# Kernel tuning notes

Measured on AMD Instinct MI355X. Metric: run time of the kernel, lower is better.

The kernel has to match this reference:

```python
import jax, jax.numpy as jnp
import numpy as np
import math

DIM = 384
NUM_HEADS = 12
WS = 8  # window_size


def setup_inputs() -> dict:
    key = jax.random.key(0)
    k1, k2, k3 = jax.random.split(key, 3)
    B, N, C = 16, 4096, DIM
    x = jax.random.normal(k1, (B, N, C), dtype=jnp.float32)
    W_qkv = jax.random.normal(k2, (C, 3 * C), dtype=jnp.float32) * 0.02
    b_qkv = jnp.zeros((3 * C,), dtype=jnp.float32)
    W_proj = jax.random.normal(k3, (C, C), dtype=jnp.float32) * 0.02
    return {"x": x, "W_qkv": W_qkv, "b_qkv": b_qkv, "W_proj": W_proj}


def window_attention(x, W_qkv, b_qkv, W_proj):
    B, N, C = x.shape
    H = W = int(math.isqrt(N))
    nh = NUM_HEADS
    hd = C // nh
    scale = hd ** (-0.5)
    ws = WS
    pad_h = (ws - H % ws) % ws
    pad_w = (ws - W % ws) % ws
    xg = x.reshape(B, H, W, C)
    if pad_h or pad_w:
        xg = jnp.pad(xg, ((0, 0), (0, pad_h), (0, pad_w), (0, 0)))
    Hp, Wp = H + pad_h, W + pad_w
    nH, nW = Hp // ws, Wp // ws
    # partition into windows: [B, nWin, ws*ws, C]
    xw = xg.reshape(B, nH, ws, nW, ws, C).transpose(0, 1, 3, 2, 4, 5)
    xw = xw.reshape(B, nH * nW, ws * ws, C)
    # qkv projection
    qkv = xw @ W_qkv + b_qkv  # [B, nWin, ws2, 3C]
    qkv = qkv.reshape(B, nH * nW, ws * ws, 3, nh, hd)
    q = qkv[..., 0, :, :].transpose(0, 1, 3, 2, 4)  # [B, nWin, nh, ws2, hd]
    k = qkv[..., 1, :, :].transpose(0, 1, 3, 2, 4)
    v = qkv[..., 2, :, :].transpose(0, 1, 3, 2, 4)
    attn = jnp.einsum('bwhqd,bwhkd->bwhqk', q, k) * scale
    attn = jax.nn.softmax(attn, axis=-1)
    out = jnp.einsum('bwhqk,bwhkd->bwhqd', attn, v)
    out = out.transpose(0, 1, 3, 2, 4).reshape(B, nH * nW, ws * ws, C)
    out = out @ W_proj
    # un-partition windows
    out = out.reshape(B, nH, nW, ws, ws, C).transpose(0, 1, 3, 2, 4, 5)
    out = out.reshape(B, Hp, Wp, C)
    if pad_h or pad_w:
        out = out[:, :H, :W, :]
    return out.reshape(B, H * W, C)


def reference(x, W_qkv, b_qkv, W_proj):
    return window_attention(x, W_qkv, b_qkv, W_proj)
```

## Files before the change

### kernel.cpp

```cpp
#include <hip/hip_runtime.h>
#include <hip/hip_bf16.h>


typedef _Float16 f16;
typedef f16 f16x8 __attribute__((ext_vector_type(8)));
typedef f16 f16x4 __attribute__((ext_vector_type(4)));
typedef float f32x4 __attribute__((ext_vector_type(4)));

#define MFMA_F16(a, b, c) __builtin_amdgcn_mfma_f32_16x16x32_f16((a), (b), (c), 0, 0, 0)

#define AS_G __attribute__((address_space(1)))
#define AS_L __attribute__((address_space(3)))
#define GLOAD_LDS16(gp, lp) \
  __builtin_amdgcn_global_load_lds((const AS_G void*)(gp), (AS_L void*)(lp), 16, 0, 0)
#define WAITVM_(N) asm volatile("s_waitcnt vmcnt(" #N ")" ::: "memory")
#define WAITVM(N) WAITVM_(N)

namespace {
constexpr int kC = 384;
constexpr int kNTok = 4096;
constexpr float kScale = 0.17677669529663687f;
constexpr int kWqPackChunks = 72 * 12 * 64;
constexpr int kWpPackChunks = 24 * 12 * 64;
constexpr size_t kWqPackBytes = (size_t)kWqPackChunks * 16;
constexpr size_t kWpPackBytes = (size_t)kWpPackChunks * 16;
constexpr size_t kQkvWsBytes = (size_t)65536 * 1152 * 2;
constexpr size_t kWsNeed = kWqPackBytes + kWpPackBytes + kQkvWsBytes;
constexpr int kQkvPackChunksFb = 6 * 12 * 12 * 64;
}


__global__ void prep_weights_split(const float* __restrict__ Wqkv,
                                   const float* __restrict__ Wproj,
                                   f16* __restrict__ wq_pack,
                                   f16* __restrict__ wp_pack) {
  int i = blockIdx.x * 256 + threadIdx.x;
  if (i < kWqPackChunks) {
    int lane = i & 63;
    int chunk = i >> 6;
    int ks = chunk % 12;
    int t = chunk / 12;
    int l15 = lane & 15, g = lane >> 4;
    int n3 = t * 16 + l15;
    int k0 = ks * 32 + g * 8;
    f16x8 v;
    #pragma unroll
    for (int j = 0; j < 8; ++j)
      v[j] = (f16)Wqkv[(size_t)(k0 + j) * (3 * kC) + n3];
    *reinterpret_cast<f16x8*>(wq_pack + (size_t)i * 8) = v;
  } else if (i < kWqPackChunks + kWpPackChunks) {
    int p = i - kWqPackChunks;
    int lane = p & 63;
    int chunk = p >> 6;
    int ks = chunk % 12;
    int t = chunk / 12;
    int l15 = lane & 15, g = lane >> 4;
    int n = t * 16 + l15;
    int k0 = ks * 32 + g * 8;
    f16x8 v;
    #pragma unroll
    for (int j = 0; j < 8; ++j)
      v[j] = (f16)Wproj[(size_t)(k0 + j) * kC + n];
    *reinterpret_cast<f16x8*>(wp_pack + (size_t)p * 8) = v;
  }
}

__global__ void prep_x(const float* __restrict__ x, f16* __restrict__ xw) {
  int c = blockIdx.x * 256 + threadIdx.x;
  int lane = c & 63;
  int t = c >> 6;
  int ks = t % 12;
  int mb = t / 12;
  int l15 = lane & 15, g = lane >> 4;
  int m = mb * 16 + l15;
  int b = m >> 12;
  int win = (m >> 6) & 63;
  int tok = m & 63;
  int n = ((win >> 3) * 8 + (tok >> 3)) * 64 + (win & 7) * 8 + (tok & 7);
  const float* src = x + ((size_t)(b << 12) + n) * kC + ks * 32 + g * 8;
  float4 v0 = *reinterpret_cast<const float4*>(src);
  float4 v1 = *reinterpret_cast<const float4*>(src + 4);
  f16x8 h = {(f16)v0.x, (f16)v0.y, (f16)v0.z, (f16)v0.w,
             (f16)v1.x, (f16)v1.y, (f16)v1.z, (f16)v1.w};
  *reinterpret_cast<f16x8*>(xw + (size_t)c * 8) = h;
}

__global__ __launch_bounds__(256, 3) void qkv_gemm2(
    const f16* __restrict__ xw, const float* __restrict__ b_qkv,
    const f16* __restrict__ wq_pack, f16* __restrict__ qkv_ws) {
  __shared__ alignas(1024) char smem[49152];

  const int tid = threadIdx.x;
  const int wid = tid >> 6;
  const int lane = tid & 63;
  const int g = lane >> 4;
  const int l15 = lane & 15;
  const int wm = wid >> 1;
  const int wn = wid & 1;

  int bid = blockIdx.x;
  int wg = (bid & 7) * 576 + (bid >> 3);
  int m_grp = wg / 9;
  int n_grp = wg - m_grp * 9;
  const int mb0 = m_grp * 8;
  const int nb0 = n_grp * 8;

  #define STAGE(KS, BUF)                                                     \
    do {                                                                     \
      const f16* ga0 = xw + (((size_t)(mb0 + wid) * 12 + (KS)) * 64 + lane) * 8;     \
      const f16* ga1 = xw + (((size_t)(mb0 + 4 + wid) * 12 + (KS)) * 64 + lane) * 8; \
      const f16* gb0 =                                                       \
          wq_pack + (((size_t)(nb0 + wid) * 12 + (KS)) * 64 + lane) * 8;     \
      const f16* gb1 =                                                       \
          wq_pack + (((size_t)(nb0 + 4 + wid) * 12 + (KS)) * 64 + lane) * 8; \
      char* la = smem + (BUF) * 16384 + wid * 1024;                          \
      char* lb = smem + (BUF) * 16384 + 8192 + wid * 1024;                   \
      GLOAD_LDS16(ga0, la);                                                  \
      GLOAD_LDS16(ga1, la + 4096);                                           \
      GLOAD_LDS16(gb0, lb);                                                  \
      GLOAD_LDS16(gb1, lb + 4096);                                           \
    } while (0)

  f32x4 acc[4][4];
  #pragma unroll
  for (int mt = 0; mt < 4; ++mt)
    #pragma unroll
    for (int nt = 0; nt < 4; ++nt) acc[mt][nt] = {0.f, 0.f, 0.f, 0.f};

  STAGE(0, 0);
  STAGE(1, 1);
  STAGE(2, 2);
  WAITVM(8);
  __builtin_amdgcn_sched_barrier(0);
  __builtin_amdgcn_s_barrier();

  #define KITER(T, ENDVM)                                                    \
    do {                                                                     \
      constexpr int buf = (T) % 3;                                           \
      f16x8 af[4], bf[4];                                                    \
      _Pragma("unroll") for (int mt = 0; mt < 4; ++mt) af[mt] =              \
          *reinterpret_cast<const f16x8*>(smem + buf * 16384 +               \
                                          (wm * 4 + mt) * 1024 + lane * 16); \
      _Pragma("unroll") for (int nt = 0; nt < 4; ++nt) bf[nt] =              \
          *reinterpret_cast<const f16x8*>(smem + buf * 16384 + 8192 +        \
                                          (wn * 4 + nt) * 1024 + lane * 16); \
      asm volatile("s_waitcnt lgkmcnt(0)" ::: "memory");                     \
      __builtin_amdgcn_sched_barrier(0);                                     \
      __builtin_amdgcn_s_barrier();                                          \
      if ((T) < 9) {                                                         \
        STAGE((T) + 3, buf);                                                 \
      }                                                                      \
      __builtin_amdgcn_s_setprio(1);                                         \
      _Pragma("unroll") for (int mt = 0; mt < 4; ++mt)                       \
          _Pragma("unroll") for (int nt = 0; nt < 4; ++nt) acc[mt][nt] =     \
          MFMA_F16(af[mt], bf[nt], acc[mt][nt]);                             \
      __builtin_amdgcn_s_setprio(0);                                         \
      WAITVM(ENDVM);                                                         \
      __builtin_amdgcn_sched_barrier(0);                                     \
      __builtin_amdgcn_s_barrier();                                          \
    } while (0)

  KITER(0, 8);
  KITER(1, 8);
  KITER(2, 8);
  KITER(3, 8);
  KITER(4, 8);
  KITER(5, 8);
  KITER(6, 8);
  KITER(7, 8);
  KITER(8, 8);
  KITER(9, 4);
  KITER(10, 0);
  KITER(11, 0);
  #undef KITER
  #undef STAGE

  f16* eo = (f16*)smem;
  #pragma unroll
  for (int nt = 0; nt < 4; ++nt) {
    int col128 = wn * 64 + nt * 16 + l15;
    float bias = b_qkv[n_grp * 128 + col128];
    int hsec_loc = col128 >> 5;
    int d = col128 & 31;
    #pragma unroll
    for (int mt = 0; mt < 4; ++mt) {
      #pragma unroll
      for (int j = 0; j < 4; ++j) {
        int tok = mt * 16 + g * 4 + j;
        eo[(((wm * 4 + hsec_loc) * 64) + tok) * 32 + d] =
            (f16)(acc[mt][nt][j] + bias);
      }
    }
  }
  __syncthreads();
  #pragma unroll
  for (int i = 0; i < 8; ++i) {
    int u = tid + i * 256;
    int win_loc = u >> 10;
    int cbl = (u >> 8) & 3;
    int inner = u & 255;
    int cb = n_grp * 4 + cbl;
    int h = cb % 12;
    int sec = cb / 12;
    size_t dst = ((size_t)(m_grp * 2 + win_loc) * 36 + h * 3 + sec) * 2048 +
                 (size_t)inner * 8;
    *reinterpret_cast<f16x8*>(qkv_ws + dst) =
        *reinterpret_cast<const f16x8*>(eo + (size_t)u * 8);
  }
}

__global__ __launch_bounds__(512, 4) void attn_proj(
    const f16* __restrict__ qkv_ws, const f16* __restrict__ wp_pack,
    float* __restrict__ out) {
  __shared__ alignas(16) f16 ao[64][392];
  __shared__ alignas(16) f16 vT[2][32][72];
  __shared__ alignas(16) f16 p_s[8][16][72];

  const int tid = threadIdx.x;
  const int wid = tid >> 6;
  const int lane = tid & 63;
  const int g = lane >> 4;
  const int l15 = lane & 15;
  const int wm = wid >> 2;
  const int wn = wid & 3;

  const int blk = blockIdx.x;
  const int b = blk >> 6;
  const int win = blk & 63;
  const int wh = win >> 3;
  const int ww = win & 7;

  const f32x4 zero4 = {0.f, 0.f, 0.f, 0.f};
  const f16* qkvb = qkv_ws + (size_t)(b * 64 + win) * 36 * 2048;

  const int v_hh = tid >> 8;
  const int v_tok = (tid >> 2) & 63;
  const int v_d0 = (tid & 3) * 8;

  for (int hp = 0; hp < 6; ++hp) {
    {
      int h2 = 2 * hp + v_hh;
      f16x8 v = *reinterpret_cast<const f16x8*>(
          qkvb + ((size_t)(h2 * 3 + 2) * 64 + v_tok) * 32 + v_d0);
      #pragma unroll
      for (int j = 0; j < 8; ++j) vT[v_hh][v_d0 + j][v_tok] = v[j];
    }
    __syncthreads();

    const int h = 2 * hp + wm;
    const f16* hb = qkvb + (size_t)h * 3 * 2048;
    f16x8 qa =
        *reinterpret_cast<const f16x8*>(hb + (wn * 16 + l15) * 32 + g * 8);
    f32x4 sacc[4];
    #pragma unroll
    for (int nt = 0; nt < 4; ++nt) sacc[nt] = zero4;
    #pragma unroll
    for (int nt = 0; nt < 4; ++nt) {
      f16x8 kb = *reinterpret_cast<const f16x8*>(
          hb + 2048 + (nt * 16 + l15) * 32 + g * 8);
      sacc[nt] = MFMA_F16(qa, kb, sacc[nt]);
    }

    float pv[4][4];
    #pragma unroll
    for (int j = 0; j < 4; ++j) {
      float m = -1e30f;
      #pragma unroll
      for (int nt = 0; nt < 4; ++nt) {
        pv[nt][j] = sacc[nt][j] * kScale;
        m = fmaxf(m, pv[nt][j]);
      }
      m = fmaxf(m, __shfl_xor(m, 1));
      m = fmaxf(m, __shfl_xor(m, 2));
      m = fmaxf(m, __shfl_xor(m, 4));
      m = fmaxf(m, __shfl_xor(m, 8));
      float s = 0.f;
      #pragma unroll
      for (int nt = 0; nt < 4; ++nt) {
        pv[nt][j] = __expf(pv[nt][j] - m);
        s += pv[nt][j];
      }
      s += __shfl_xor(s, 1);
      s += __shfl_xor(s, 2);
      s += __shfl_xor(s, 4);
      s += __shfl_xor(s, 8);
      float inv = 1.0f / s;
      #pragma unroll
      for (int nt = 0; nt < 4; ++nt)
        p_s[wid][g * 4 + j][nt * 16 + l15] = (f16)(pv[nt][j] * inv);
    }

    f32x4 oacc[2];
    oacc[0] = zero4;
    oacc[1] = zero4;
    #pragma unroll
    for (int ks = 0; ks < 2; ++ks) {
      f16x8 pa =
          *reinterpret_cast<const f16x8*>(&p_s[wid][l15][ks * 32 + g * 8]);
      #pragma unroll
      for (int nt = 0; nt < 2; ++nt) {
        f16x8 vb = *reinterpret_cast<const f16x8*>(
            &vT[wm][nt * 16 + l15][ks * 32 + g * 8]);
        oacc[nt] = MFMA_F16(pa, vb, oacc[nt]);
      }
    }
    #pragma unroll
    for (int nt = 0; nt < 2; ++nt)
      #pragma unroll
      for (int j = 0; j < 4; ++j)
        ao[wn * 16 + g * 4 + j][h * 32 + nt * 16 + l15] = (f16)oacc[nt][j];
    __syncthreads();
  }

  f32x4 pacc[2][6];
  #pragma unroll
  for (int mt = 0; mt < 2; ++mt)
    #pragma unroll
    for (int nt = 0; nt < 6; ++nt) pacc[mt][nt] = zero4;

  const f16* pptr[6];
  #pragma unroll
  for (int nt = 0; nt < 6; ++nt) {
    int t = wn * 6 + nt;
    pptr[nt] = wp_pack + ((size_t)(t * 12) * 64 + lane) * 8;
  }
  f16x8 pbf[2][6];
  #pragma unroll
  for (int nt = 0; nt < 6; ++nt)
    pbf[0][nt] = *reinterpret_cast<const f16x8*>(pptr[nt]);

  #pragma unroll
  for (int ks = 0; ks < 12; ++ks) {
    const int cur = ks & 1;
    if (ks < 11) {
      #pragma unroll
      for (int nt = 0; nt < 6; ++nt)
        pbf[cur ^ 1][nt] =
            *reinterpret_cast<const f16x8*>(pptr[nt] + (ks + 1) * 512);
    }
    f16x8 paf[2];
    #pragma unroll
    for (int mt = 0; mt < 2; ++mt)
      paf[mt] = *reinterpret_cast<const f16x8*>(
          &ao[wm * 32 + mt * 16 + l15][ks * 32 + g * 8]);
    #pragma unroll
    for (int mt = 0; mt < 2; ++mt)
      #pragma unroll
      for (int nt = 0; nt < 6; ++nt)
        pacc[mt][nt] = MFMA_F16(paf[mt], pbf[cur][nt], pacc[mt][nt]);
  }

  const size_t outbase = (size_t)b * kNTok * kC;
  #pragma unroll
  for (int mt = 0; mt < 2; ++mt) {
    #pragma unroll
    for (int j = 0; j < 4; ++j) {
      int r = wm * 32 + mt * 16 + g * 4 + j;
      int n = (wh * 8 + (r >> 3)) * 64 + ww * 8 + (r & 7);
      float* orow = out + outbase + (size_t)n * kC + wn * 96;
      #pragma unroll
      for (int nt = 0; nt < 6; ++nt) orow[nt * 16 + l15] = pacc[mt][nt][j];
    }
  }
}


__global__ void prep_weights_fb(const float* __restrict__ Wqkv,
                                const float* __restrict__ Wproj,
                                f16* __restrict__ wq_pack,
                                f16* __restrict__ wp_pack) {
  int i = blockIdx.x * 256 + threadIdx.x;
  if (i < kQkvPackChunksFb) {
    int lane = i & 63;
    int chunk = i >> 6;
    int ks = chunk % 12;
    int t = (chunk / 12) % 12;
    int hp = chunk / 144;
    int l15 = lane & 15, g = lane >> 4;
    int base = t * 16;
    int hh = base / 96;
    int cc = base - hh * 96;
    int sec = cc >> 5;
    int dbhi = cc & 31;
    int n3 = sec * kC + (2 * hp + hh) * 32 + dbhi + l15;
    int k0 = ks * 32 + g * 8;
    f16x8 v;
    #pragma unroll
    for (int j = 0; j < 8; ++j)
      v[j] = (f16)Wqkv[(size_t)(k0 + j) * (3 * kC) + n3];
    *reinterpret_cast<f16x8*>(wq_pack + (size_t)i * 8) = v;
  } else if (i < kQkvPackChunksFb + kWpPackChunks) {
    int p = i - kQkvPackChunksFb;
    int lane = p & 63;
    int chunk = p >> 6;
    int ks = chunk % 12;
    int t = chunk / 12;
    int l15 = lane & 15, g = lane >> 4;
    int n = t * 16 + l15;
    int k0 = ks * 32 + g * 8;
    f16x8 v;
    #pragma unroll
    for (int j = 0; j < 8; ++j)
      v[j] = (f16)Wproj[(size_t)(k0 + j) * kC + n];
    *reinterpret_cast<f16x8*>(wp_pack + (size_t)p * 8) = v;
  }
}

__global__ __launch_bounds__(512, 2) void win_attn_fused_fb(
    const float* __restrict__ x, const float* __restrict__ b_qkv,
    const f16* __restrict__ wq_pack, const f16* __restrict__ wp_pack,
    float* __restrict__ out) {
  __shared__ alignas(16) f16 xs[64][392];
  __shared__ alignas(16) f16 ao[64][392];
  __shared__ alignas(16) f16 q_s[2][64][40];
  __shared__ alignas(16) f16 k_s[2][64][40];
  __shared__ alignas(16) f16 vT[2][32][72];
  __shared__ alignas(16) f16 p_s[8][16][72];

  const int tid = threadIdx.x;
  const int wid = tid >> 6;
  const int lane = tid & 63;
  const int g = lane >> 4;
  const int l15 = lane & 15;
  const int wm = wid >> 2;
  const int wn = wid & 3;

  const int blk = blockIdx.x;
  const int b = blk >> 6;
  const int win = blk & 63;
  const int wh = win >> 3;
  const int ww = win & 7;

  const f32x4 zero4 = {0.f, 0.f, 0.f, 0.f};

  {
    const float* xb = x + (size_t)b * kNTok * kC;
    #pragma unroll
    for (int it = 0; it < 12; ++it) {
      int idx = tid + it * 512;
      int r = idx / 96;
      int c4 = idx - r * 96;
      int n = (wh * 8 + (r >> 3)) * 64 + ww * 8 + (r & 7);
      float4 v = *reinterpret_cast<const float4*>(xb + (size_t)n * kC + c4 * 4);
      f16x4 hv = {(f16)v.x, (f16)v.y, (f16)v.z, (f16)v.w};
      *reinterpret_cast<f16x4*>(&xs[r][c4 * 4]) = hv;
    }
  }
  __syncthreads();

  for (int hp = 0; hp < 6; ++hp) {
    f32x4 acc[2][3];
    #pragma unroll
    for (int mt = 0; mt < 2; ++mt)
      #pragma unroll
      for (int nt = 0; nt < 3; ++nt) acc[mt][nt] = zero4;

    const f16* bptr[3];
    int secv[3], dbv[3], hhv[3];
    #pragma unroll
    for (int nt = 0; nt < 3; ++nt) {
      int t = wn * 3 + nt;
      int base = t * 16;
      int hh = base / 96;
      int cc = base - hh * 96;
      hhv[nt] = hh;
      secv[nt] = cc >> 5;
      dbv[nt] = cc & 31;
      bptr[nt] = wq_pack + ((size_t)((hp * 12 + t) * 12) * 64 + lane) * 8;
    }

    f16x8 bf[4][3];
    f16x8 af[2][2];
    #pragma unroll
    for (int p = 0; p < 3; ++p)
      #pragma unroll
      for (int nt = 0; nt < 3; ++nt)
        bf[p][nt] = *reinterpret_cast<const f16x8*>(bptr[nt] + p * 512);
    #pragma unroll
    for (int mt = 0; mt < 2; ++mt)
      af[0][mt] = *reinterpret_cast<const f16x8*>(
          &xs[wm * 32 + mt * 16 + l15][g * 8]);

    #pragma unroll
    for (int ks = 0; ks < 12; ++ks) {
      const int cur = ks & 3;
      const int ca = ks & 1;
      if (ks < 9) {
        const int nx = (ks + 3) & 3;
        #pragma unroll
        for (int nt = 0; nt < 3; ++nt)
          bf[nx][nt] =
              *reinterpret_cast<const f16x8*>(bptr[nt] + (ks + 3) * 512);
      }
      if (ks < 11) {
        #pragma unroll
        for (int mt = 0; mt < 2; ++mt)
          af[ca ^ 1][mt] = *reinterpret_cast<const f16x8*>(
              &xs[wm * 32 + mt * 16 + l15][(ks + 1) * 32 + g * 8]);
      }
      #pragma unroll
      for (int mt = 0; mt < 2; ++mt)
        #pragma unroll
        for (int nt = 0; nt < 3; ++nt)
          acc[mt][nt] = MFMA_F16(af[ca][mt], bf[cur][nt], acc[mt][nt]);
    }

    #pragma unroll
    for (int nt = 0; nt < 3; ++nt) {
      int hh = hhv[nt], sec = secv[nt];
      int col = dbv[nt] + l15;
      float bias = b_qkv[sec * kC + (2 * hp + hh) * 32 + col];
      #pragma unroll
      for (int mt = 0; mt < 2; ++mt) {
        #pragma unroll
        for (int j = 0; j < 4; ++j) {
          int r = wm * 32 + mt * 16 + g * 4 + j;
          f16 hv = (f16)(acc[mt][nt][j] + bias);
          if (sec == 0) q_s[hh][r][col] = hv;
          else if (sec == 1) k_s[hh][r][col] = hv;
          else vT[hh][col][r] = hv;
        }
      }
    }
    __syncthreads();

    f32x4 sacc[4];
    #pragma unroll
    for (int nt = 0; nt < 4; ++nt) sacc[nt] = zero4;
    f16x8 qa = *reinterpret_cast<const f16x8*>(&q_s[wm][wn * 16 + l15][g * 8]);
    #pragma unroll
    for (int nt = 0; nt < 4; ++nt) {
      f16x8 kb =
          *reinterpret_cast<const f16x8*>(&k_s[wm][nt * 16 + l15][g * 8]);
      sacc[nt] = MFMA_F16(qa, kb, sacc[nt]);
    }

    float pv[4][4];
    #pragma unroll
    for (int j = 0; j < 4; ++j) {
      float m = -1e30f;
      #pragma unroll
      for (int nt = 0; nt < 4; ++nt) {
        pv[nt][j] = sacc[nt][j] * kScale;
        m = fmaxf(m, pv[nt][j]);
      }
      m = fmaxf(m, __shfl_xor(m, 1));
      m = fmaxf(m, __shfl_xor(m, 2));
      m = fmaxf(m, __shfl_xor(m, 4));
      m = fmaxf(m, __shfl_xor(m, 8));
      float s = 0.f;
      #pragma unroll
      for (int nt = 0; nt < 4; ++nt) {
        pv[nt][j] = __expf(pv[nt][j] - m);
        s += pv[nt][j];
      }
      s += __shfl_xor(s, 1);
      s += __shfl_xor(s, 2);
      s += __shfl_xor(s, 4);
      s += __shfl_xor(s, 8);
      float inv = 1.0f / s;
      #pragma unroll
      for (int nt = 0; nt < 4; ++nt)
        p_s[wid][g * 4 + j][nt * 16 + l15] = (f16)(pv[nt][j] * inv);
    }

    f32x4 oacc[2];
    oacc[0] = zero4;
    oacc[1] = zero4;
    #pragma unroll
    for (int ks = 0; ks < 2; ++ks) {
      f16x8 pa =
          *reinterpret_cast<const f16x8*>(&p_s[wid][l15][ks * 32 + g * 8]);
      #pragma unroll
      for (int nt = 0; nt < 2; ++nt) {
        f16x8 vb = *reinterpret_cast<const f16x8*>(
            &vT[wm][nt * 16 + l15][ks * 32 + g * 8]);
        oacc[nt] = MFMA_F16(pa, vb, oacc[nt]);
      }
    }
    #pragma unroll
    for (int nt = 0; nt < 2; ++nt)
      #pragma unroll
      for (int j = 0; j < 4; ++j)
        ao[wn * 16 + g * 4 + j][(2 * hp + wm) * 32 + nt * 16 + l15] =
            (f16)oacc[nt][j];
    __syncthreads();
  }

  f32x4 pacc[2][6];
  #pragma unroll
  for (int mt = 0; mt < 2; ++mt)
    #pragma unroll
    for (int nt = 0; nt < 6; ++nt) pacc[mt][nt] = zero4;

  const f16* pptr[6];
  #pragma unroll
  for (int nt = 0; nt < 6; ++nt) {
    int t = wn * 6 + nt;
    pptr[nt] = wp_pack + ((size_t)(t * 12) * 64 + lane) * 8;
  }
  f16x8 pbf[3][6];
  f16x8 paf[2][2];
  #pragma unroll
  for (int p = 0; p < 2; ++p)
    #pragma unroll
    for (int nt = 0; nt < 6; ++nt)
      pbf[p][nt] = *reinterpret_cast<const f16x8*>(pptr[nt] + p * 512);
  #pragma unroll
  for (int mt = 0; mt < 2; ++mt)
    paf[0][mt] =
        *reinterpret_cast<const f16x8*>(&ao[wm * 32 + mt * 16 + l15][g * 8]);

  #pragma unroll
  for (int ks = 0; ks < 12; ++ks) {
    const int cur = ks % 3;
    const int ca = ks & 1;
    if (ks < 10) {
      const int nx = (ks + 2) % 3;
      #pragma unroll
      for (int nt = 0; nt < 6; ++nt)
        pbf[nx][nt] =
            *reinterpret_cast<const f16x8*>(pptr[nt] + (ks + 2) * 512);
    }
    if (ks < 11) {
      #pragma unroll
      for (int mt = 0; mt < 2; ++mt)
        paf[ca ^ 1][mt] = *reinterpret_cast<const f16x8*>(
            &ao[wm * 32 + mt * 16 + l15][(ks + 1) * 32 + g * 8]);
    }
    #pragma unroll
    for (int mt = 0; mt < 2; ++mt)
      #pragma unroll
      for (int nt = 0; nt < 6; ++nt)
        pacc[mt][nt] = MFMA_F16(paf[ca][mt], pbf[cur][nt], pacc[mt][nt]);
  }

  const size_t outbase = (size_t)b * kNTok * kC;
  #pragma unroll
  for (int mt = 0; mt < 2; ++mt) {
    #pragma unroll
    for (int j = 0; j < 4; ++j) {
      int r = wm * 32 + mt * 16 + g * 4 + j;
      int n = (wh * 8 + (r >> 3)) * 64 + ww * 8 + (r & 7);
      float* orow = out + outbase + (size_t)n * kC + wn * 96;
      #pragma unroll
      for (int nt = 0; nt < 6; ++nt) orow[nt * 16 + l15] = pacc[mt][nt][j];
    }
  }
}


extern "C" void kernel_launch(void* const* d_in, const int* in_sizes, int n_in,
                              void* d_out, int out_size, void* d_ws,
                              size_t ws_size, hipStream_t stream) {
  const float* x = (const float*)d_in[0];
  const float* Wqkv = (const float*)d_in[1];
  const float* bqkv = (const float*)d_in[2];
  const float* Wproj = (const float*)d_in[3];
  float* out = (float*)d_out;

  if (ws_size >= kWsNeed) {
    f16* wq_pack = (f16*)d_ws;
    f16* wp_pack = (f16*)((char*)d_ws + kWqPackBytes);
    f16* qkv_ws = (f16*)((char*)d_ws + kWqPackBytes + kWpPackBytes);
    f16* xw = (f16*)d_out;

    int prep_threads = kWqPackChunks + kWpPackChunks;
    hipLaunchKernelGGL(prep_weights_split, dim3((prep_threads + 255) / 256),
                       dim3(256), 0, stream, Wqkv, Wproj, wq_pack, wp_pack);
    hipLaunchKernelGGL(prep_x, dim3(12288), dim3(256), 0, stream, x, xw);
    hipLaunchKernelGGL(qkv_gemm2, dim3(4608), dim3(256), 0, stream, xw, bqkv,
                       wq_pack, qkv_ws);
    hipLaunchKernelGGL(attn_proj, dim3(16 * 64), dim3(512), 0, stream, qkv_ws,
                       wp_pack, out);
  } else {
    f16* wq_pack = (f16*)d_ws;
    f16* wp_pack = (f16*)((char*)d_ws + (size_t)kQkvPackChunksFb * 16);
    int prep_threads = kQkvPackChunksFb + kWpPackChunks;
    hipLaunchKernelGGL(prep_weights_fb, dim3((prep_threads + 255) / 256),
                       dim3(256), 0, stream, Wqkv, Wproj, wq_pack, wp_pack);
    hipLaunchKernelGGL(win_attn_fused_fb, dim3(16 * 64), dim3(512), 0, stream,
                       x, bqkv, wq_pack, wp_pack, out);
  }
}
```

Measured before the change: 173.9 us.

## Pre-transpose V in QKV epilogue and restructure attention as one wave per head

The QKV GEMM epilogue now writes V transposed (d-major, with an XOR swizzle in shared memory), so the attention kernel can load V fragments straight from global memory without an LDS transpose. The attention kernel is rewritten to use 12 waves (768 threads), one per head, computing all 64 query rows per wave with registers only, which removes five of the six per-head-pair barrier rounds. Block indices are also remapped for better locality. The trade-off is higher register pressure per wave and lower occupancy per CU (launch bounds 768,2).

Measured after the change: 184.1 us. 1.06x slower.

```diff
diff --git a/kernel.cpp b/kernel.cpp
--- a/kernel.cpp
+++ b/kernel.cpp
@@ -180,15 +180,20 @@
   for (int nt = 0; nt < 4; ++nt) {
     int col128 = wn * 64 + nt * 16 + l15;
     float bias = b_qkv[n_grp * 128 + col128];
-    int hsec_loc = col128 >> 5;
+    int hsec_loc = wn * 2 + (nt >> 1);
     int d = col128 & 31;
+    int sec = (n_grp * 4 + hsec_loc) / 12;
+    int base = (wm * 4 + hsec_loc) * 2048;
     #pragma unroll
     for (int mt = 0; mt < 4; ++mt) {
       #pragma unroll
       for (int j = 0; j < 4; ++j) {
         int tok = mt * 16 + g * 4 + j;
-        eo[(((wm * 4 + hsec_loc) * 64) + tok) * 32 + d] =
-            (f16)(acc[mt][nt][j] + bias);
+        f16 hv = (f16)(acc[mt][nt][j] + bias);
+        if (sec == 2)
+          eo[base + d * 64 + (tok ^ ((d & 7) << 3))] = hv;
+        else
+          eo[base + tok * 32 + d] = hv;
       }
     }
   }
@@ -204,70 +209,81 @@
     int sec = cb / 12;
     size_t dst = ((size_t)(m_grp * 2 + win_loc) * 36 + h * 3 + sec) * 2048 +
                  (size_t)inner * 8;
-    *reinterpret_cast<f16x8*>(qkv_ws + dst) =
-        *reinterpret_cast<const f16x8*>(eo + (size_t)u * 8);
-  }
-}
-
-__global__ __launch_bounds__(512, 4) void attn_proj(
+    f16x8 hv;
+    if (sec == 2) {
+      int d = inner >> 3;
+      int t0 = inner & 7;
+      hv = *reinterpret_cast<const f16x8*>(
+          eo + (win_loc * 4 + cbl) * 2048 + d * 64 + ((t0 * 8) ^ ((d & 7) << 3)));
+    } else {
+      hv = *reinterpret_cast<const f16x8*>(eo + (size_t)u * 8);
+    }
+    *reinterpret_cast<f16x8*>(qkv_ws + dst) = hv;
+  }
+}
+
+__global__ __launch_bounds__(768, 2) void attn_proj2(
     const f16* __restrict__ qkv_ws, const f16* __restrict__ wp_pack,
     float* __restrict__ out) {
   __shared__ alignas(16) f16 ao[64][392];
-  __shared__ alignas(16) f16 vT[2][32][72];
-  __shared__ alignas(16) f16 p_s[8][16][72];
+  __shared__ alignas(16) f16 p_s[12][16][68];
 
   const int tid = threadIdx.x;
   const int wid = tid >> 6;
   const int lane = tid & 63;
   const int g = lane >> 4;
   const int l15 = lane & 15;
-  const int wm = wid >> 2;
-  const int wn = wid & 3;
-
-  const int blk = blockIdx.x;
+
+  int blk = (int)blockIdx.x;
+  blk = (blk & 7) * 128 + (blk >> 3);
   const int b = blk >> 6;
   const int win = blk & 63;
   const int wh = win >> 3;
   const int ww = win & 7;
 
   const f32x4 zero4 = {0.f, 0.f, 0.f, 0.f};
-  const f16* qkvb = qkv_ws + (size_t)(b * 64 + win) * 36 * 2048;
-
-  const int v_hh = tid >> 8;
-  const int v_tok = (tid >> 2) & 63;
-  const int v_d0 = (tid & 3) * 8;
-
-  for (int hp = 0; hp < 6; ++hp) {
-    {
-      int h2 = 2 * hp + v_hh;
-      f16x8 v = *reinterpret_cast<const f16x8*>(
-          qkvb + ((size_t)(h2 * 3 + 2) * 64 + v_tok) * 32 + v_d0);
-      #pragma unroll
-      for (int j = 0; j < 8; ++j) vT[v_hh][v_d0 + j][v_tok] = v[j];
-    }
-    __syncthreads();
-
-    const int h = 2 * hp + wm;
-    const f16* hb = qkvb + (size_t)h * 3 * 2048;
-    f16x8 qa =
-        *reinterpret_cast<const f16x8*>(hb + (wn * 16 + l15) * 32 + g * 8);
-    f32x4 sacc[4];
-    #pragma unroll
-    for (int nt = 0; nt < 4; ++nt) sacc[nt] = zero4;
-    #pragma unroll
-    for (int nt = 0; nt < 4; ++nt) {
-      f16x8 kb = *reinterpret_cast<const f16x8*>(
-          hb + 2048 + (nt * 16 + l15) * 32 + g * 8);
-      sacc[nt] = MFMA_F16(qa, kb, sacc[nt]);
-    }
-
+  const f16* hb = qkv_ws + ((size_t)(b * 64 + win) * 36 + wid * 3) * 2048;
+
+  f16x8 qf[4], kf[4], vf[2][2];
+  #pragma unroll
+  for (int mt = 0; mt < 4; ++mt)
+    qf[mt] = *reinterpret_cast<const f16x8*>(hb + (mt * 16 + l15) * 32 + g * 8);
+  #pragma unroll
+  for (int nt = 0; nt < 4; ++nt)
+    kf[nt] = *reinterpret_cast<const f16x8*>(hb + 2048 + (nt * 16 + l15) * 32 + g * 8);
+  #pragma unroll
+  for (int ntd = 0; ntd < 2; ++ntd)
+    #pragma unroll
+    for (int ks = 0; ks < 2; ++ks)
+      vf[ntd][ks] = *reinterpret_cast<const f16x8*>(
+          hb + 4096 + (ntd * 16 + l15) * 64 + ks * 32 + g * 8);
+
+  f32x4 sacc[4][4];
+  #pragma unroll
+  for (int mt = 0; mt < 4; ++mt)
+    #pragma unroll
+    for (int nt = 0; nt < 4; ++nt) sacc[mt][nt] = zero4;
+  #pragma unroll
+  for (int mt = 0; mt < 4; ++mt)
+    #pragma unroll
+    for (int nt = 0; nt < 4; ++nt)
+      sacc[mt][nt] = MFMA_F16(qf[mt], kf[nt], sacc[mt][nt]);
+
+  f32x4 oacc[4][2];
+  #pragma unroll
+  for (int mt = 0; mt < 4; ++mt) {
+    oacc[mt][0] = zero4;
+    oacc[mt][1] = zero4;
+  }
+  #pragma unroll
+  for (int mt = 0; mt < 4; ++mt) {
     float pv[4][4];
     #pragma unroll
     for (int j = 0; j < 4; ++j) {
       float m = -1e30f;
       #pragma unroll
       for (int nt = 0; nt < 4; ++nt) {
-        pv[nt][j] = sacc[nt][j] * kScale;
+        pv[nt][j] = sacc[mt][nt][j] * kScale;
         m = fmaxf(m, pv[nt][j]);
       }
       m = fmaxf(m, __shfl_xor(m, 1));
@@ -289,44 +305,38 @@
       for (int nt = 0; nt < 4; ++nt)
         p_s[wid][g * 4 + j][nt * 16 + l15] = (f16)(pv[nt][j] * inv);
     }
-
-    f32x4 oacc[2];
-    oacc[0] = zero4;
-    oacc[1] = zero4;
     #pragma unroll
     for (int ks = 0; ks < 2; ++ks) {
       f16x8 pa =
           *reinterpret_cast<const f16x8*>(&p_s[wid][l15][ks * 32 + g * 8]);
       #pragma unroll
-      for (int nt = 0; nt < 2; ++nt) {
-        f16x8 vb = *reinterpret_cast<const f16x8*>(
-            &vT[wm][nt * 16 + l15][ks * 32 + g * 8]);
-        oacc[nt] = MFMA_F16(pa, vb, oacc[nt]);
-      }
-    }
-    #pragma unroll
-    for (int nt = 0; nt < 2; ++nt)
+      for (int ntd = 0; ntd < 2; ++ntd)
+        oacc[mt][ntd] = MFMA_F16(pa, vf[ntd][ks], oacc[mt][ntd]);
+    }
+    #pragma unroll
+    for (int ntd = 0; ntd < 2; ++ntd)
       #pragma unroll
       for (int j = 0; j < 4; ++j)
-        ao[wn * 16 + g * 4 + j][h * 32 + nt * 16 + l15] = (f16)oacc[nt][j];
-    __syncthreads();
-  }
-
-  f32x4 pacc[2][6];
-  #pragma unroll
-  for (int mt = 0; mt < 2; ++mt)
-    #pragma unroll
-    for (int nt = 0; nt < 6; ++nt) pacc[mt][nt] = zero4;
-
-  const f16* pptr[6];
-  #pragma unroll
-  for (int nt = 0; nt < 6; ++nt) {
-    int t = wn * 6 + nt;
+        ao[mt * 16 + g * 4 + j][wid * 32 + ntd * 16 + l15] =
+            (f16)oacc[mt][ntd][j];
+  }
+  __syncthreads();
+
+  f32x4 pacc[4][2];
+  #pragma unroll
+  for (int mt = 0; mt < 4; ++mt) {
+    pacc[mt][0] = zero4;
+    pacc[mt][1] = zero4;
+  }
+  const f16* pptr[2];
+  #pragma unroll
+  for (int nt = 0; nt < 2; ++nt) {
+    int t = wid * 2 + nt;
     pptr[nt] = wp_pack + ((size_t)(t * 12) * 64 + lane) * 8;
   }
-  f16x8 pbf[2][6];
-  #pragma unroll
-  for (int nt = 0; nt < 6; ++nt)
+  f16x8 pbf[2][2];
+  #pragma unroll
+  for (int nt = 0; nt < 2; ++nt)
     pbf[0][nt] = *reinterpret_cast<const f16x8*>(pptr[nt]);
 
   #pragma unroll
@@ -334,32 +344,32 @@
     const int cur = ks & 1;
     if (ks < 11) {
       #pragma unroll
-      for (int nt = 0; nt < 6; ++nt)
+      for (int nt = 0; nt < 2; ++nt)
         pbf[cur ^ 1][nt] =
             *reinterpret_cast<const f16x8*>(pptr[nt] + (ks + 1) * 512);
     }
-    f16x8 paf[2];
-    #pragma unroll
-    for (int mt = 0; mt < 2; ++mt)
+    f16x8 paf[4];
+    #pragma unroll
+    for (int mt = 0; mt < 4; ++mt)
       paf[mt] = *reinterpret_cast<const f16x8*>(
-          &ao[wm * 32 + mt * 16 + l15][ks * 32 + g * 8]);
-    #pragma unroll
-    for (int mt = 0; mt < 2; ++mt)
-      #pragma unroll
-      for (int nt = 0; nt < 6; ++nt)
+          &ao[mt * 16 + l15][ks * 32 + g * 8]);
+    #pragma unroll
+    for (int mt = 0; mt < 4; ++mt)
+      #pragma unroll
+      for (int nt = 0; nt < 2; ++nt)
         pacc[mt][nt] = MFMA_F16(paf[mt], pbf[cur][nt], pacc[mt][nt]);
   }
 
   const size_t outbase = (size_t)b * kNTok * kC;
   #pragma unroll
-  for (int mt = 0; mt < 2; ++mt) {
+  for (int mt = 0; mt < 4; ++mt) {
     #pragma unroll
     for (int j = 0; j < 4; ++j) {
-      int r = wm * 32 + mt * 16 + g * 4 + j;
+      int r = mt * 16 + g * 4 + j;
       int n = (wh * 8 + (r >> 3)) * 64 + ww * 8 + (r & 7);
-      float* orow = out + outbase + (size_t)n * kC + wn * 96;
-      #pragma unroll
-      for (int nt = 0; nt < 6; ++nt) orow[nt * 16 + l15] = pacc[mt][nt][j];
+      float* orow = out + outbase + (size_t)n * kC + wid * 32;
+      #pragma unroll
+      for (int nt = 0; nt < 2; ++nt) orow[nt * 16 + l15] = pacc[mt][nt][j];
     }
   }
 }
@@ -671,7 +681,7 @@
     hipLaunchKernelGGL(prep_x, dim3(12288), dim3(256), 0, stream, x, xw);
     hipLaunchKernelGGL(qkv_gemm2, dim3(4608), dim3(256), 0, stream, xw, bqkv,
                        wq_pack, qkv_ws);
-    hipLaunchKernelGGL(attn_proj, dim3(16 * 64), dim3(512), 0, stream, qkv_ws,
+    hipLaunchKernelGGL(attn_proj2, dim3(16 * 64), dim3(768), 0, stream, qkv_ws,
                        wp_pack, out);
   } else {
     f16* wq_pack = (f16*)d_ws;
```
